# Performance work log

Hardware: AMD Instinct MI355X
Metric: run time of the kernel (lower is better)

The kernel has to match this reference:

```python
import jax, jax.numpy as jnp
import numpy as np

D_MODEL = 768
D_INNER = 1536   # expand=2
D_STATE = 16
D_CONV = 4
DT_RANK = 48     # ceil(768/16)
B, T, N = 2, 4, 196


def _rmsnorm(x, w, eps=1e-5):
    var = jnp.mean(x * x, axis=-1, keepdims=True)
    return x * jax.lax.rsqrt(var + eps) * w


def _causal_dwconv(x, w, b):
    # x: (b, l, di), w: (di, k) depthwise, causal left-pad k-1
    xc = jnp.swapaxes(x, 1, 2)  # (b, di, l)
    out = jax.lax.conv_general_dilated(
        xc, w[:, None, :], window_strides=(1,), padding=[(D_CONV - 1, 0)],
        feature_group_count=D_INNER, dimension_numbers=('NCH', 'OIH', 'NCH'))
    return jnp.swapaxes(out + b[None, :, None], 1, 2)


def _selective_scan(u, dt, A, Bm, Cm, Dp):
    # u, dt: (b,l,di); Bm, Cm: (b,l,n); A: (di,n); Dp: (di,)
    dA = jnp.exp(dt[..., None] * A)                    # (b,l,di,n)
    dBu = (dt * u)[..., None] * Bm[:, :, None, :]      # (b,l,di,n)

    def step(h, inp):
        dA_t, dBu_t, C_t = inp
        h = dA_t * h + dBu_t                           # (b,di,n)
        return h, jnp.einsum('bdn,bn->bd', h, C_t)

    h0 = jnp.zeros((u.shape[0], D_INNER, D_STATE), u.dtype)
    _, ys = jax.lax.scan(step, h0, (jnp.swapaxes(dA, 0, 1),
                                    jnp.swapaxes(dBu, 0, 1),
                                    jnp.swapaxes(Cm, 0, 1)))
    return jnp.swapaxes(ys, 0, 1) + u * Dp


def _mamba(x, in_w, cw, cb, xp_w, dt_w, dt_b, A_log, Dp, out_w):
    xz = jnp.einsum('blc,ec->ble', x, in_w)            # (b,l,2*di)
    xb, z = jnp.split(xz, 2, axis=-1)
    xb = jax.nn.silu(_causal_dwconv(xb, cw, cb))
    x_dbl = jnp.einsum('bld,ed->ble', xb, xp_w)        # (b,l,dt_rank+2n)
    dt, Bm, Cm = jnp.split(x_dbl, [DT_RANK, DT_RANK + D_STATE], axis=-1)
    dt = jax.nn.softplus(jnp.einsum('blr,dr->bld', dt, dt_w) + dt_b)
    y = _selective_scan(xb, dt, -jnp.exp(A_log), Bm, Cm, Dp)
    y = y * jax.nn.silu(z)
    return jnp.einsum('bld,cd->blc', y, out_w)


def _block(x, i, norm_w, in_proj_w, conv_w, conv_b, x_proj_w, dt_proj_w,
           dt_proj_b, A_log, D, mix_out_w):
    # residual Mamba block: x + mixer(norm(x)); zero-initialized ssm/conv state
    return x + _mamba(_rmsnorm(x, norm_w[i]), in_proj_w[i], conv_w[i], conv_b[i],
                      x_proj_w[i], dt_proj_w[i], dt_proj_b[i], A_log[i], D[i],
                      mix_out_w[i])


def _bimamba(x, norm_w, in_proj_w, conv_w, conv_b, x_proj_w, dt_proj_w,
             dt_proj_b, A_log, D, mix_out_w, gate_w, gate_b, proj_w, proj_b):
    b, t, n, c = x.shape
    xs = x.reshape(b, t * n, c)
    params = (norm_w, in_proj_w, conv_w, conv_b, x_proj_w, dt_proj_w,
              dt_proj_b, A_log, D, mix_out_w)
    out_f = _block(xs, 0, *params)
    flip_t = lambda y: y.reshape(b, t, n, c)[:, ::-1].reshape(b, t * n, c)
    out_b = flip_t(_block(flip_t(xs), 1, *params))
    gate = jax.nn.sigmoid(
        jnp.einsum('blc,dc->bld', jnp.concatenate([out_f, out_b], -1), gate_w)
        + gate_b)
    out = gate * out_f + (1.0 - gate) * out_b
    out = jnp.einsum('bld,cd->blc', out, proj_w) + proj_b
    return out.reshape(b, t, n, c)


def setup_inputs() -> dict:
    key = jax.random.key(0)
    ks = jax.random.split(key, 12)
    s = 0.02
    a_log = jnp.broadcast_to(
        jnp.log(jnp.arange(1, D_STATE + 1, dtype=jnp.float32)),
        (2, D_INNER, D_STATE)).copy()
    return {
        'x': jax.random.normal(ks[0], (B, T, N, D_MODEL), jnp.float32),
        'norm_w': jnp.ones((2, D_MODEL), jnp.float32),
        'in_proj_w': jax.random.normal(ks[1], (2, 2 * D_INNER, D_MODEL), jnp.float32) * s,
        'conv_w': jax.random.normal(ks[2], (2, D_INNER, D_CONV), jnp.float32) * 0.2,
        'conv_b': jnp.zeros((2, D_INNER), jnp.float32),
        'x_proj_w': jax.random.normal(ks[3], (2, DT_RANK + 2 * D_STATE, D_INNER), jnp.float32) * s,
        'dt_proj_w': jax.random.normal(ks[4], (2, D_INNER, DT_RANK), jnp.float32) * s,
        'dt_proj_b': jax.random.normal(ks[5], (2, D_INNER), jnp.float32) * 0.5 - 4.0,
        'A_log': a_log,
        'D': jnp.ones((2, D_INNER), jnp.float32),
        'mix_out_w': jax.random.normal(ks[6], (2, D_MODEL, D_INNER), jnp.float32) * s,
        'gate_w': jax.random.normal(ks[7], (D_MODEL, 2 * D_MODEL), jnp.float32) * s,
        'gate_b': jnp.zeros((D_MODEL,), jnp.float32),
        'proj_w': jax.random.normal(ks[8], (D_MODEL, D_MODEL), jnp.float32) * s,
        'proj_b': jnp.zeros((D_MODEL,), jnp.float32),
    }


def reference(x, norm_w, in_proj_w, conv_w, conv_b, x_proj_w, dt_proj_w,
              dt_proj_b, A_log, D, mix_out_w, gate_w, gate_b, proj_w, proj_b):
    return _bimamba(x, norm_w, in_proj_w, conv_w, conv_b, x_proj_w, dt_proj_w,
                    dt_proj_b, A_log, D, mix_out_w, gate_w, gate_b, proj_w,
                    proj_b)
```

## Files before the change

kernel.cpp:

```cpp
#include <hip/hip_runtime.h>
#include <cstdint>
#include <cstddef>

#define BB 2
#define TT 4
#define NN 196
#define LL (TT*NN)
#define BLr (BB*LL)
#define CM 768
#define DI 1536
#define DS 16
#define DTR 48
#define XD 80
#define GCH 16
#define LC (LL/GCH)
#define NST (2*BB*DI*DS)

typedef short s16x8 __attribute__((ext_vector_type(8)));
typedef float f32x4 __attribute__((ext_vector_type(4)));

static __device__ __forceinline__ float sigmoidf_(float x) {
  return 1.f / (1.f + __expf(-x));
}
static __device__ __forceinline__ unsigned short f2bf(float f) {
  unsigned int u = __float_as_uint(f);
  unsigned int r = (u + 0x7fffu + ((u >> 16) & 1u)) >> 16;
  return (unsigned short)r;
}
static __device__ __forceinline__ float bf2f(unsigned short u) {
  return __uint_as_float(((unsigned int)u) << 16);
}
static __device__ __forceinline__ float softplusf_(float v) {
  return (v > 20.f) ? v : __logf(1.f + __expf(v));
}
static __device__ __forceinline__ void gload_lds16(const void* g, void* l) {
  __builtin_amdgcn_global_load_lds(
      (const __attribute__((address_space(1))) void*)g,
      (__attribute__((address_space(3))) void*)l, 16, 0, 0);
}

__global__ __launch_bounds__(256) void rmsnorm_k(const float* __restrict__ x,
    const float* __restrict__ nw, unsigned short* __restrict__ xn)
{
  int blk = blockIdx.x;
  int l   = blk % LL;
  int b   = (blk / LL) % BB;
  int dir = blk / (BB*LL);
  int lsrc = l;
  if (dir == 1) { int t = l / NN, n = l % NN; lsrc = (TT-1-t)*NN + n; }
  const float* xp = x + ((size_t)b*LL + lsrc)*CM;
  float s = 0.f;
  for (int c = threadIdx.x; c < CM; c += 256) { float v = xp[c]; s += v*v; }
  #pragma unroll
  for (int off = 32; off > 0; off >>= 1) s += __shfl_down(s, off);
  __shared__ float red[4];
  if ((threadIdx.x & 63) == 0) red[threadIdx.x >> 6] = s;
  __syncthreads();
  float tot = red[0] + red[1] + red[2] + red[3];
  float r = rsqrtf(tot * (1.f/CM) + 1e-5f);
  const float* w = nw + dir*CM;
  unsigned short* o = xn + (size_t)blk*CM;
  for (int c = threadIdx.x; c < CM; c += 256) o[c] = f2bf(xp[c] * r * w[c]);
}

#define S_INW  4718592
#define S_OUTW 2359296
#define S_GATW 1179648
#define S_PRJW 589824
#define S_XPW  245760
#define S_DTW  196608
#define E0 S_INW
#define E1 (E0 + S_OUTW)
#define E2 (E1 + S_GATW)
#define E3 (E2 + S_PRJW)
#define E4 (E3 + S_XPW)
#define E5 (E4 + S_DTW)
__global__ void multicast_k(const float* __restrict__ in_w,
    const float* __restrict__ out_w, const float* __restrict__ gate_w,
    const float* __restrict__ proj_w, const float* __restrict__ xp_w,
    const float* __restrict__ dt_w, unsigned short* __restrict__ dst)
{
  int i = blockIdx.x*256 + threadIdx.x;
  if (i >= E5) return;
  float v;
  if (i < E0)       v = in_w[i];
  else if (i < E1)  v = out_w[i - E0];
  else if (i < E2)  v = gate_w[i - E1];
  else if (i < E3)  v = proj_w[i - E2];
  else if (i < E4)  v = xp_w[i - E3];
  else {
    int j = i - E4, r = j >> 6, c = j & 63;
    v = (c < 48) ? dt_w[r*48 + c] : 0.f;
  }
  dst[i] = f2bf(v);
}

template <int BM, int BN>
__device__ __forceinline__ void gemm_core(
    const unsigned short* __restrict__ A, int lda,
    const unsigned short* __restrict__ W, int ldw,
    int M, int N, int K, int m0, int n0,
    short* As, short* Ws, f32x4 (*acc)[BN/32])
{
  const int tid = threadIdx.x;
  const int wv = tid >> 6, lane = tid & 63;
  const int wm0 = (wv >> 1)*(BM/2), wn0 = (wv & 1)*(BN/2);
  const int lm = lane & 15, g = lane >> 4;
  const int r8 = lane >> 3, ch = lane & 7;
  const int chs = ch ^ r8;
  constexpr int MT = BM/32, NT = BN/32;
  for (int k0 = 0; k0 < K; k0 += 64) {
    #pragma unroll
    for (int e = 0; e < BM/32; ++e) {
      int rb = e*32 + wv*8;
      int gr = m0 + rb + r8; if (gr >= M) gr = M - 1;
      gload_lds16(A + (size_t)gr*lda + k0 + chs*8, &As[rb*64 + lane*8]);
    }
    #pragma unroll
    for (int e = 0; e < BN/32; ++e) {
      int rb = e*32 + wv*8;
      int gn = n0 + rb + r8; if (gn >= N) gn = N - 1;
      gload_lds16(W + (size_t)gn*ldw + k0 + chs*8, &Ws[rb*64 + lane*8]);
    }
    __syncthreads();
    #pragma unroll
    for (int s = 0; s < 2; ++s) {
      s16x8 af[MT], bf[NT];
      #pragma unroll
      for (int i = 0; i < MT; ++i) {
        int R = wm0 + i*16 + lm;
        af[i] = *(const s16x8*)(&As[R*64 + (((s*4 + g) ^ (R & 7))*8)]);
      }
      #pragma unroll
      for (int j = 0; j < NT; ++j) {
        int Rn = wn0 + j*16 + lm;
        bf[j] = *(const s16x8*)(&Ws[Rn*64 + (((s*4 + g) ^ (Rn & 7))*8)]);
      }
      #pragma unroll
      for (int i = 0; i < MT; ++i)
        #pragma unroll
        for (int j = 0; j < NT; ++j)
          acc[i][j] = __builtin_amdgcn_mfma_f32_16x16x32_bf16(af[i], bf[j], acc[i][j], 0, 0, 0);
    }
    __syncthreads();
  }
}

__global__ __launch_bounds__(256, 4) void gemm_in_k(
    const unsigned short* __restrict__ xn, const unsigned short* __restrict__ w,
    unsigned short* __restrict__ xzout)
{
  __shared__ short As[64*64];
  __shared__ short Ws[128*64];
  const int dir = blockIdx.z;
  const unsigned short* A = xn + (size_t)dir*BLr*CM;
  const unsigned short* W = w  + (size_t)dir*2*DI*CM;
  unsigned short* C = xzout + (size_t)dir*BLr*2*DI;
  const int m0 = blockIdx.y*64, n0 = blockIdx.x*128;
  f32x4 acc[2][4];
  #pragma unroll
  for (int i = 0; i < 2; ++i)
    #pragma unroll
    for (int j = 0; j < 4; ++j) acc[i][j] = (f32x4){0.f,0.f,0.f,0.f};
  gemm_core<64,128>(A, CM, W, CM, BLr, 2*DI, CM, m0, n0, As, Ws, acc);
  const int tid = threadIdx.x, wv = tid >> 6, lane = tid & 63;
  const int wm0 = (wv >> 1)*32, wn0 = (wv & 1)*64;
  const int lm = lane & 15, g = lane >> 4;
  #pragma unroll
  for (int i = 0; i < 2; ++i) {
    int row = m0 + wm0 + i*16 + g*4;
    #pragma unroll
    for (int j = 0; j < 4; ++j) {
      int col = n0 + wn0 + j*16 + lm;
      #pragma unroll
      for (int r = 0; r < 4; ++r)
        if (row + r < BLr) C[(size_t)(row + r)*2*DI + col] = f2bf(acc[i][j][r]);
    }
  }
}

__global__ __launch_bounds__(256, 4) void gemm_dt_k(
    const unsigned short* __restrict__ xdblb, const unsigned short* __restrict__ w,
    const float* __restrict__ dtb, float* __restrict__ dtv)
{
  __shared__ short As[64*64];
  __shared__ short Ws[128*64];
  const int dir = blockIdx.z;
  const unsigned short* A = xdblb + (size_t)dir*BLr*64;
  const unsigned short* W = w + (size_t)dir*DI*64;
  float* C = dtv + (size_t)dir*BLr*DI;
  const float* bias = dtb + (size_t)dir*DI;
  const int m0 = blockIdx.y*64, n0 = blockIdx.x*128;
  f32x4 acc[2][4];
  #pragma unroll
  for (int i = 0; i < 2; ++i)
    #pragma unroll
    for (int j = 0; j < 4; ++j) acc[i][j] = (f32x4){0.f,0.f,0.f,0.f};
  gemm_core<64,128>(A, 64, W, 64, BLr, DI, 64, m0, n0, As, Ws, acc);
  const int tid = threadIdx.x, wv = tid >> 6, lane = tid & 63;
  const int wm0 = (wv >> 1)*32, wn0 = (wv & 1)*64;
  const int lm = lane & 15, g = lane >> 4;
  #pragma unroll
  for (int i = 0; i < 2; ++i) {
    int row = m0 + wm0 + i*16 + g*4;
    #pragma unroll
    for (int j = 0; j < 4; ++j) {
      int col = n0 + wn0 + j*16 + lm;
      float bv = bias[col];
      #pragma unroll
      for (int r = 0; r < 4; ++r) {
        if (row + r >= BLr) continue;
        C[(size_t)(row + r)*DI + col] = softplusf_(acc[i][j][r] + bv);
      }
    }
  }
}

__global__ __launch_bounds__(256, 4) void gemm_outp_k(
    const unsigned short* __restrict__ yb, const unsigned short* __restrict__ w,
    const float* __restrict__ x, float* __restrict__ fbuf,
    float* __restrict__ bbuf, unsigned short* __restrict__ cat)
{
  __shared__ short As[64*64];
  __shared__ short Ws[64*64];
  const int dir = blockIdx.z;
  const unsigned short* A = yb + (size_t)dir*BLr*DI;
  const unsigned short* W = w + (size_t)dir*CM*DI;
  const int m0 = blockIdx.y*64, n0 = blockIdx.x*64;
  f32x4 acc[2][2];
  #pragma unroll
  for (int i = 0; i < 2; ++i)
    #pragma unroll
    for (int j = 0; j < 2; ++j) acc[i][j] = (f32x4){0.f,0.f,0.f,0.f};
  gemm_core<64,64>(A, DI, W, DI, BLr, CM, DI, m0, n0, As, Ws, acc);
  const int tid = threadIdx.x, wv = tid >> 6, lane = tid & 63;
  const int wm0 = (wv >> 1)*32, wn0 = (wv & 1)*32;
  const int lm = lane & 15, g = lane >> 4;
  #pragma unroll
  for (int i = 0; i < 2; ++i) {
    int row = m0 + wm0 + i*16 + g*4;
    #pragma unroll
    for (int j = 0; j < 2; ++j) {
      int col = n0 + wn0 + j*16 + lm;
      #pragma unroll
      for (int r = 0; r < 4; ++r) {
        int rr = row + r;
        if (rr >= BLr) continue;
        int rt = rr;
        if (dir == 1) {
          int l = rr % LL, b = rr / LL;
          int t = l / NN, nn = l % NN;
          rt = b*LL + (TT-1-t)*NN + nn;
        }
        float v = x[(size_t)rt*CM + col] + acc[i][j][r];
        if (dir == 0) {
          fbuf[(size_t)rt*CM + col] = v;
          cat[(size_t)rt*(2*CM) + col] = f2bf(v);
        } else {
          bbuf[(size_t)rt*CM + col] = v;
          cat[(size_t)rt*(2*CM) + CM + col] = f2bf(v);
        }
      }
    }
  }
}

__global__ __launch_bounds__(256, 4) void gemm_gate_k(
    const unsigned short* __restrict__ cat, const unsigned short* __restrict__ w,
    const float* __restrict__ gb, const float* __restrict__ fbuf,
    const float* __restrict__ bbuf, unsigned short* __restrict__ mixb)
{
  __shared__ short As[64*64];
  __shared__ short Ws[64*64];
  const int m0 = blockIdx.y*64, n0 = blockIdx.x*64;
  f32x4 acc[2][2];
  #pragma unroll
  for (int i = 0; i < 2; ++i)
    #pragma unroll
    for (int j = 0; j < 2; ++j) acc[i][j] = (f32x4){0.f,0.f,0.f,0.f};
  gemm_core<64,64>(cat, 2*CM, w, 2*CM, BLr, CM, 2*CM, m0, n0, As, Ws, acc);
  const int tid = threadIdx.x, wv = tid >> 6, lane = tid & 63;
  const int wm0 = (wv >> 1)*32, wn0 = (wv & 1)*32;
  const int lm = lane & 15, g = lane >> 4;
  #pragma unroll
  for (int i = 0; i < 2; ++i) {
    int row = m0 + wm0 + i*16 + g*4;
    #pragma unroll
    for (int j = 0; j < 2; ++j) {
      int col = n0 + wn0 + j*16 + lm;
      float bv = gb[col];
      #pragma unroll
      for (int r = 0; r < 4; ++r) {
        int rr = row + r;
        if (rr >= BLr) continue;
        float gg = sigmoidf_(acc[i][j][r] + bv);
        float fv = fbuf[(size_t)rr*CM + col];
        float bo = bbuf[(size_t)rr*CM + col];
        mixb[(size_t)rr*CM + col] = f2bf(gg*fv + (1.f - gg)*bo);
      }
    }
  }
}

__global__ __launch_bounds__(256, 4) void gemm_proj_k(
    const unsigned short* __restrict__ mixb, const unsigned short* __restrict__ w,
    const float* __restrict__ pb, float* __restrict__ out)
{
  __shared__ short As[64*64];
  __shared__ short Ws[64*64];
  const int m0 = blockIdx.y*64, n0 = blockIdx.x*64;
  f32x4 acc[2][2];
  #pragma unroll
  for (int i = 0; i < 2; ++i)
    #pragma unroll
    for (int j = 0; j < 2; ++j) acc[i][j] = (f32x4){0.f,0.f,0.f,0.f};
  gemm_core<64,64>(mixb, CM, w, CM, BLr, CM, CM, m0, n0, As, Ws, acc);
  const int tid = threadIdx.x, wv = tid >> 6, lane = tid & 63;
  const int wm0 = (wv >> 1)*32, wn0 = (wv & 1)*32;
  const int lm = lane & 15, g = lane >> 4;
  #pragma unroll
  for (int i = 0; i < 2; ++i) {
    int row = m0 + wm0 + i*16 + g*4;
    #pragma unroll
    for (int j = 0; j < 2; ++j) {
      int col = n0 + wn0 + j*16 + lm;
      float bv = pb[col];
      #pragma unroll
      for (int r = 0; r < 4; ++r)
        if (row + r < BLr) out[(size_t)(row + r)*CM + col] = acc[i][j][r] + bv;
    }
  }
}

__global__ __launch_bounds__(256, 2) void gemm_xproj(
    const unsigned short* __restrict__ ub, const unsigned short* __restrict__ xpw,
    float* __restrict__ part)
{
  __shared__ short As[128*64];
  __shared__ short Ws[128*64];
  const int ks = blockIdx.x, mt = blockIdx.y, dir = blockIdx.z;
  const unsigned short* A = ub + (size_t)dir*BLr*DI + ks*(DI/8);
  const unsigned short* W = xpw + (size_t)dir*XD*DI + ks*(DI/8);
  const int m0 = mt*128;
  f32x4 acc[4][4];
  #pragma unroll
  for (int i = 0; i < 4; ++i)
    #pragma unroll
    for (int j = 0; j < 4; ++j) acc[i][j] = (f32x4){0.f,0.f,0.f,0.f};
  gemm_core<128,128>(A, DI, W, DI, BLr, XD, DI/8, m0, 0, As, Ws, acc);
  const int tid = threadIdx.x, wv = tid >> 6, lane = tid & 63;
  const int wm0 = (wv >> 1)*64, wn0 = (wv & 1)*64;
  const int lm = lane & 15, g = lane >> 4;
  float* P = part + ((size_t)(dir*8 + ks)*BLr)*XD;
  #pragma unroll
  for (int i = 0; i < 4; ++i) {
    int row = m0 + wm0 + i*16 + g*4;
    #pragma unroll
    for (int j = 0; j < 4; ++j) {
      int col = wn0 + j*16 + lm;
      if (col >= XD) continue;
      #pragma unroll
      for (int r = 0; r < 4; ++r)
        if (row + r < BLr) P[(size_t)(row + r)*XD + col] = acc[i][j][r];
    }
  }
}

__global__ void xreduce_k(const float* __restrict__ part,
    float* __restrict__ xdbl, unsigned short* __restrict__ xdbl_b)
{
  int i = blockIdx.x*256 + threadIdx.x;
  if (i >= 2*BLr*XD) return;
  int c = i % XD;
  int r = i / XD;
  int dir = r / BLr, row = r % BLr;
  float s = 0.f;
  #pragma unroll
  for (int ks = 0; ks < 8; ++ks)
    s += part[((size_t)(dir*8 + ks)*BLr + row)*XD + c];
  xdbl[(size_t)r*XD + c] = s;
  if (c < DTR)      xdbl_b[(size_t)r*64 + c] = f2bf(s);
  else if (c < 64)  xdbl_b[(size_t)r*64 + c] = 0;
}

__global__ __launch_bounds__(256) void conv_silu_k(
    const unsigned short* __restrict__ xz, const float* __restrict__ cw,
    const float* __restrict__ cb, unsigned short* __restrict__ ub)
{
  size_t idx = (size_t)blockIdx.x*256 + threadIdx.x;
  if (idx >= (size_t)2*BLr*DI) return;
  int di  = (int)(idx % DI);
  size_t r = idx / DI;
  int l   = (int)(r % LL);
  int dir = (int)(r / (BB*LL));
  size_t rowbase = r - l;
  const float* w = cw + ((size_t)dir*DI + di)*4;
  float acc = cb[dir*DI + di];
  #pragma unroll
  for (int k = 0; k < 4; ++k) {
    int lp = l - 3 + k;
    if (lp >= 0) acc = fmaf(w[k], bf2f(xz[(rowbase + lp)*(2*DI) + di]), acc);
  }
  float v = acc * sigmoidf_(acc);
  ub[idx] = f2bf(v);
}

__global__ __launch_bounds__(256) void scanA_k(const float* __restrict__ dtv,
    const unsigned short* __restrict__ u, const float* __restrict__ xdbl,
    const float* __restrict__ A_log, float* __restrict__ carry,
    float* __restrict__ Pm)
{
  int bx = blockIdx.x;
  int g = bx & (GCH-1);
  int rest = bx / GCH;
  int dchunk = rest % (DI/64);
  int b   = (rest / (DI/64)) % BB;
  int dir = rest / ((DI/64)*BB);
  int tid = threadIdx.x;
  int dl = tid >> 2, q = tid & 3;
  int d = dchunk*64 + dl;
  size_t rb = ((size_t)dir*BB + b) * LL + (size_t)g*LC;
  const float* dtp = dtv + rb*DI + d;
  const unsigned short* up = u + rb*DI + d;
  const float* xB  = xdbl + rb*XD + DTR + 4*q;
  f32x4 al = *(const f32x4*)(A_log + ((size_t)dir*DI + d)*DS + 4*q);
  float Av[4];
  #pragma unroll
  for (int i = 0; i < 4; ++i) Av[i] = -__expf(al[i]);
  float h[4] = {0.f,0.f,0.f,0.f};
  float S = 0.f;
  float ndt[2], nu[2]; f32x4 nB[2];
  #pragma unroll
  for (int e = 0; e < 2; ++e) {
    ndt[e] = dtp[(size_t)e*DI];
    nu[e]  = bf2f(up[(size_t)e*DI]);
    nB[e]  = *(const f32x4*)(xB + (size_t)e*XD);
  }
  #pragma unroll 2
  for (int j = 0; j < LC; ++j) {
    int s = j & 1;
    float cdt = ndt[s], cu = nu[s];
    f32x4 cB = nB[s];
    int lp = j + 2;
    if (lp < LC) {
      ndt[s] = dtp[(size_t)lp*DI];
      nu[s]  = bf2f(up[(size_t)lp*DI]);
      nB[s]  = *(const f32x4*)(xB + (size_t)lp*XD);
    }
    float du = cdt * cu;
    S += cdt;
    #pragma unroll
    for (int i = 0; i < 4; ++i) {
      float dA = __expf(cdt * Av[i]);
      h[i] = fmaf(dA, h[i], du * cB[i]);
    }
  }
  size_t sid = (((size_t)(dir*BB + b)*DI + d)*DS + 4*q);
  f32x4 hc = {h[0], h[1], h[2], h[3]};
  f32x4 pc = {__expf(Av[0]*S), __expf(Av[1]*S), __expf(Av[2]*S), __expf(Av[3]*S)};
  *(f32x4*)(carry + (size_t)g*NST + sid) = hc;
  *(f32x4*)(Pm    + (size_t)g*NST + sid) = pc;
}

__global__ __launch_bounds__(256) void scanB_k(float* __restrict__ carry,
    const float* __restrict__ Pm)
{
  int sid = blockIdx.x*256 + threadIdx.x;
  float h = 0.f;
  #pragma unroll
  for (int g = 0; g < GCH; ++g) {
    float c = carry[(size_t)g*NST + sid];
    float p = Pm[(size_t)g*NST + sid];
    carry[(size_t)g*NST + sid] = h;
    h = fmaf(p, h, c);
  }
}

__global__ __launch_bounds__(256) void scanC_k(const float* __restrict__ dtv,
    const unsigned short* __restrict__ u, const unsigned short* __restrict__ xz,
    const float* __restrict__ xdbl, const float* __restrict__ A_log,
    const float* __restrict__ Dp, const float* __restrict__ h_in,
    unsigned short* __restrict__ y)
{
  int bx = blockIdx.x;
  int g = bx & (GCH-1);
  int rest = bx / GCH;
  int dchunk = rest % (DI/64);
  int b   = (rest / (DI/64)) % BB;
  int dir = rest / ((DI/64)*BB);
  int tid = threadIdx.x;
  int dl = tid >> 2, q = tid & 3;
  int d = dchunk*64 + dl;
  size_t rb = ((size_t)dir*BB + b) * LL + (size_t)g*LC;
  const float* dtp = dtv + rb*DI + d;
  const unsigned short* up = u + rb*DI + d;
  const unsigned short* zp = xz + rb*(2*DI) + DI + d;
  const float* xB  = xdbl + rb*XD + DTR + 4*q;
  const float* xC  = xB + DS;
  unsigned short* yp = y + rb*DI + d;
  f32x4 al = *(const f32x4*)(A_log + ((size_t)dir*DI + d)*DS + 4*q);
  float Av[4];
  #pragma unroll
  for (int i = 0; i < 4; ++i) Av[i] = -__expf(al[i]);
  float Dd = Dp[dir*DI + d];
  size_t sid = (((size_t)(dir*BB + b)*DI + d)*DS + 4*q);
  f32x4 h4 = *(const f32x4*)(h_in + (size_t)g*NST + sid);
  float h[4] = {h4[0], h4[1], h4[2], h4[3]};
  float ndt[2], nu[2], nz[2]; f32x4 nB[2], nC[2];
  #pragma unroll
  for (int e = 0; e < 2; ++e) {
    ndt[e] = dtp[(size_t)e*DI];
    nu[e]  = bf2f(up[(size_t)e*DI]);
    nz[e]  = bf2f(zp[(size_t)e*(2*DI)]);
    nB[e]  = *(const f32x4*)(xB + (size_t)e*XD);
    nC[e]  = *(const f32x4*)(xC + (size_t)e*XD);
  }
  #pragma unroll 2
  for (int j = 0; j < LC; ++j) {
    int s = j & 1;
    float cdt = ndt[s], cu = nu[s], cz = nz[s];
    f32x4 cB = nB[s], cC = nC[s];
    int lp = j + 2;
    if (lp < LC) {
      ndt[s] = dtp[(size_t)lp*DI];
      nu[s]  = bf2f(up[(size_t)lp*DI]);
      nz[s]  = bf2f(zp[(size_t)lp*(2*DI)]);
      nB[s]  = *(const f32x4*)(xB + (size_t)lp*XD);
      nC[s]  = *(const f32x4*)(xC + (size_t)lp*XD);
    }
    float du = cdt * cu;
    float acc = 0.f;
    #pragma unroll
    for (int i = 0; i < 4; ++i) {
      float dA = __expf(cdt * Av[i]);
      h[i] = fmaf(dA, h[i], du * cB[i]);
      acc = fmaf(h[i], cC[i], acc);
    }
    acc += __shfl_xor(acc, 1);
    acc += __shfl_xor(acc, 2);
    if (q == 0) {
      float yv = (acc + cu * Dd) * (cz * sigmoidf_(cz));
      yp[(size_t)j*DI] = f2bf(yv);
    }
  }
}

extern "C" void kernel_launch(void* const* d_in, const int* in_sizes, int n_in,
                              void* d_out, int out_size, void* d_ws, size_t ws_size,
                              hipStream_t stream)
{
  (void)in_sizes; (void)n_in; (void)out_size; (void)ws_size;
  const float* x      = (const float*)d_in[0];
  const float* norm_w = (const float*)d_in[1];
  const float* in_w   = (const float*)d_in[2];
  const float* conv_w = (const float*)d_in[3];
  const float* conv_b = (const float*)d_in[4];
  const float* xp_w   = (const float*)d_in[5];
  const float* dt_w   = (const float*)d_in[6];
  const float* dt_b   = (const float*)d_in[7];
  const float* A_log  = (const float*)d_in[8];
  const float* Dp     = (const float*)d_in[9];
  const float* out_w  = (const float*)d_in[10];
  const float* gate_w = (const float*)d_in[11];
  const float* gate_b = (const float*)d_in[12];
  const float* proj_w = (const float*)d_in[13];
  const float* proj_b = (const float*)d_in[14];
  float* out = (float*)d_out;
  char* wsb  = (char*)d_ws;

  unsigned short* w_all   = (unsigned short*)(wsb + 0);
  unsigned short* in_w_b  = w_all;
  unsigned short* out_w_b = w_all + E0;
  unsigned short* gate_w_b= w_all + E1;
  unsigned short* proj_w_b= w_all + E2;
  unsigned short* xp_w_b  = w_all + E3;
  unsigned short* dt_w_b  = w_all + E4;
  unsigned short* xz_b = (unsigned short*)(wsb + 18579456);
  unsigned short* ub   = (unsigned short*)(wsb + 37847040);
  float* xdbl  = (float*)(wsb + 57114624);
  float* dtvb  = (float*)(wsb + 58118144);
  unsigned short* y_b = (unsigned short*)(wsb + 77385728);
  unsigned short* tmp = (unsigned short*)(wsb + 87019520);
  float* fbuf  = (float*)(wsb + 96653312);
  float* bbuf  = (float*)(wsb + 101470208);
  unsigned short* cat_b = (unsigned short*)(wsb + 106287104);
  unsigned short* mix_b = (unsigned short*)(wsb + 111104000);

  unsigned short* xn_b   = tmp;
  unsigned short* xdbl_b = tmp;
  float* part  = (float*)(wsb + 0);
  float* carry = (float*)(wsb + 0);
  float* Pmat  = (float*)(wsb + 87019520 + 524288);

  rmsnorm_k<<<2*BLr, 256, 0, stream>>>(x, norm_w, xn_b);
  multicast_k<<<(E5 + 255)/256, 256, 0, stream>>>(
      in_w, out_w, gate_w, proj_w, xp_w, dt_w, w_all);
  gemm_in_k<<<dim3(3072/128, (BLr+63)/64, 2), 256, 0, stream>>>(
      xn_b, in_w_b, xz_b);
  conv_silu_k<<<(int)(((size_t)2*BLr*DI + 255)/256), 256, 0, stream>>>(
      xz_b, conv_w, conv_b, ub);
  gemm_xproj<<<dim3(8, (BLr+127)/128, 2), 256, 0, stream>>>(ub, xp_w_b, part);
  xreduce_k<<<(2*BLr*XD + 255)/256, 256, 0, stream>>>(part, xdbl, xdbl_b);
  gemm_dt_k<<<dim3(DI/128, (BLr+63)/64, 2), 256, 0, stream>>>(
      xdbl_b, dt_w_b, dt_b, dtvb);
  scanA_k<<<2*BB*(DI/64)*GCH, 256, 0, stream>>>(
      dtvb, ub, xdbl, A_log, carry, Pmat);
  scanB_k<<<NST/256, 256, 0, stream>>>(carry, Pmat);
  scanC_k<<<2*BB*(DI/64)*GCH, 256, 0, stream>>>(
      dtvb, ub, xz_b, xdbl, A_log, Dp, carry, y_b);
  gemm_outp_k<<<dim3(CM/64, (BLr+63)/64, 2), 256, 0, stream>>>(
      y_b, out_w_b, x, fbuf, bbuf, cat_b);
  gemm_gate_k<<<dim3(CM/64, (BLr+63)/64, 1), 256, 0, stream>>>(
      cat_b, gate_w_b, gate_b, fbuf, bbuf, mix_b);
  gemm_proj_k<<<dim3(CM/64, (BLr+63)/64, 1), 256, 0, stream>>>(
      mix_b, proj_w_b, proj_b, out);
}
```

Baseline: 310.0 us.

## Fuse rmsnorm with weight cast, enlarge GEMM tiles, drop fp32 residual buffers

Merges the rmsnorm and weight bf16-cast kernels into one launch. Grows the in-projection GEMM tile to 128x128 with launch bounds lowered to 2, and widens the out-projection tile to 64x128. Removes the fp32 forward/backward residual buffers, so the gate kernel reads the bf16 concatenated values instead. That cuts memory traffic and a launch, but the gating now uses bf16-rounded branch outputs, a small precision change.

Measured after the change: 310.2 us. Within noise of the previous version (+0.1%).

```diff
diff --git a/kernel.cpp b/kernel.cpp
--- a/kernel.cpp
+++ b/kernel.cpp
@@ -39,30 +39,6 @@
       (__attribute__((address_space(3))) void*)l, 16, 0, 0);
 }
 
-__global__ __launch_bounds__(256) void rmsnorm_k(const float* __restrict__ x,
-    const float* __restrict__ nw, unsigned short* __restrict__ xn)
-{
-  int blk = blockIdx.x;
-  int l   = blk % LL;
-  int b   = (blk / LL) % BB;
-  int dir = blk / (BB*LL);
-  int lsrc = l;
-  if (dir == 1) { int t = l / NN, n = l % NN; lsrc = (TT-1-t)*NN + n; }
-  const float* xp = x + ((size_t)b*LL + lsrc)*CM;
-  float s = 0.f;
-  for (int c = threadIdx.x; c < CM; c += 256) { float v = xp[c]; s += v*v; }
-  #pragma unroll
-  for (int off = 32; off > 0; off >>= 1) s += __shfl_down(s, off);
-  __shared__ float red[4];
-  if ((threadIdx.x & 63) == 0) red[threadIdx.x >> 6] = s;
-  __syncthreads();
-  float tot = red[0] + red[1] + red[2] + red[3];
-  float r = rsqrtf(tot * (1.f/CM) + 1e-5f);
-  const float* w = nw + dir*CM;
-  unsigned short* o = xn + (size_t)blk*CM;
-  for (int c = threadIdx.x; c < CM; c += 256) o[c] = f2bf(xp[c] * r * w[c]);
-}
-
 #define S_INW  4718592
 #define S_OUTW 2359296
 #define S_GATW 1179648
@@ -75,24 +51,49 @@
 #define E3 (E2 + S_PRJW)
 #define E4 (E3 + S_XPW)
 #define E5 (E4 + S_DTW)
-__global__ void multicast_k(const float* __restrict__ in_w,
-    const float* __restrict__ out_w, const float* __restrict__ gate_w,
-    const float* __restrict__ proj_w, const float* __restrict__ xp_w,
-    const float* __restrict__ dt_w, unsigned short* __restrict__ dst)
-{
-  int i = blockIdx.x*256 + threadIdx.x;
-  if (i >= E5) return;
-  float v;
-  if (i < E0)       v = in_w[i];
-  else if (i < E1)  v = out_w[i - E0];
-  else if (i < E2)  v = gate_w[i - E1];
-  else if (i < E3)  v = proj_w[i - E2];
-  else if (i < E4)  v = xp_w[i - E3];
-  else {
-    int j = i - E4, r = j >> 6, c = j & 63;
-    v = (c < 48) ? dt_w[r*48 + c] : 0.f;
-  }
-  dst[i] = f2bf(v);
+#define NCAST ((E5)/256)
+
+__global__ __launch_bounds__(256) void pre_k(const float* __restrict__ x,
+    const float* __restrict__ nw, unsigned short* __restrict__ xn,
+    const float* __restrict__ in_w, const float* __restrict__ out_w,
+    const float* __restrict__ gate_w, const float* __restrict__ proj_w,
+    const float* __restrict__ xp_w, const float* __restrict__ dt_w,
+    unsigned short* __restrict__ dst)
+{
+  int blk = blockIdx.x;
+  if (blk < 2*BLr) {
+    int l   = blk % LL;
+    int b   = (blk / LL) % BB;
+    int dir = blk / (BB*LL);
+    int lsrc = l;
+    if (dir == 1) { int t = l / NN, n = l % NN; lsrc = (TT-1-t)*NN + n; }
+    const float* xp = x + ((size_t)b*LL + lsrc)*CM;
+    float s = 0.f;
+    for (int c = threadIdx.x; c < CM; c += 256) { float v = xp[c]; s += v*v; }
+    #pragma unroll
+    for (int off = 32; off > 0; off >>= 1) s += __shfl_down(s, off);
+    __shared__ float red[4];
+    if ((threadIdx.x & 63) == 0) red[threadIdx.x >> 6] = s;
+    __syncthreads();
+    float tot = red[0] + red[1] + red[2] + red[3];
+    float r = rsqrtf(tot * (1.f/CM) + 1e-5f);
+    const float* w = nw + dir*CM;
+    unsigned short* o = xn + (size_t)blk*CM;
+    for (int c = threadIdx.x; c < CM; c += 256) o[c] = f2bf(xp[c] * r * w[c]);
+  } else {
+    int i = (blk - 2*BLr)*256 + threadIdx.x;
+    float v;
+    if (i < E0)       v = in_w[i];
+    else if (i < E1)  v = out_w[i - E0];
+    else if (i < E2)  v = gate_w[i - E1];
+    else if (i < E3)  v = proj_w[i - E2];
+    else if (i < E4)  v = xp_w[i - E3];
+    else {
+      int j = i - E4, r = j >> 6, c = j & 63;
+      v = (c < 48) ? dt_w[r*48 + c] : 0.f;
+    }
+    dst[i] = f2bf(v);
+  }
 }
 
 template <int BM, int BN>
@@ -146,28 +147,28 @@
   }
 }
 
-__global__ __launch_bounds__(256, 4) void gemm_in_k(
+__global__ __launch_bounds__(256, 2) void gemm_in_k(
     const unsigned short* __restrict__ xn, const unsigned short* __restrict__ w,
     unsigned short* __restrict__ xzout)
 {
-  __shared__ short As[64*64];
+  __shared__ short As[128*64];
   __shared__ short Ws[128*64];
   const int dir = blockIdx.z;
   const unsigned short* A = xn + (size_t)dir*BLr*CM;
   const unsigned short* W = w  + (size_t)dir*2*DI*CM;
   unsigned short* C = xzout + (size_t)dir*BLr*2*DI;
-  const int m0 = blockIdx.y*64, n0 = blockIdx.x*128;
-  f32x4 acc[2][4];
-  #pragma unroll
-  for (int i = 0; i < 2; ++i)
+  const int m0 = blockIdx.y*128, n0 = blockIdx.x*128;
+  f32x4 acc[4][4];
+  #pragma unroll
+  for (int i = 0; i < 4; ++i)
     #pragma unroll
     for (int j = 0; j < 4; ++j) acc[i][j] = (f32x4){0.f,0.f,0.f,0.f};
-  gemm_core<64,128>(A, CM, W, CM, BLr, 2*DI, CM, m0, n0, As, Ws, acc);
+  gemm_core<128,128>(A, CM, W, CM, BLr, 2*DI, CM, m0, n0, As, Ws, acc);
   const int tid = threadIdx.x, wv = tid >> 6, lane = tid & 63;
-  const int wm0 = (wv >> 1)*32, wn0 = (wv & 1)*64;
+  const int wm0 = (wv >> 1)*64, wn0 = (wv & 1)*64;
   const int lm = lane & 15, g = lane >> 4;
   #pragma unroll
-  for (int i = 0; i < 2; ++i) {
+  for (int i = 0; i < 4; ++i) {
     int row = m0 + wm0 + i*16 + g*4;
     #pragma unroll
     for (int j = 0; j < 4; ++j) {
@@ -218,29 +219,28 @@
 
 __global__ __launch_bounds__(256, 4) void gemm_outp_k(
     const unsigned short* __restrict__ yb, const unsigned short* __restrict__ w,
-    const float* __restrict__ x, float* __restrict__ fbuf,
-    float* __restrict__ bbuf, unsigned short* __restrict__ cat)
+    const float* __restrict__ x, unsigned short* __restrict__ cat)
 {
   __shared__ short As[64*64];
-  __shared__ short Ws[64*64];
+  __shared__ short Ws[128*64];
   const int dir = blockIdx.z;
   const unsigned short* A = yb + (size_t)dir*BLr*DI;
   const unsigned short* W = w + (size_t)dir*CM*DI;
-  const int m0 = blockIdx.y*64, n0 = blockIdx.x*64;
-  f32x4 acc[2][2];
+  const int m0 = blockIdx.y*64, n0 = blockIdx.x*128;
+  f32x4 acc[2][4];
   #pragma unroll
   for (int i = 0; i < 2; ++i)
     #pragma unroll
-    for (int j = 0; j < 2; ++j) acc[i][j] = (f32x4){0.f,0.f,0.f,0.f};
-  gemm_core<64,64>(A, DI, W, DI, BLr, CM, DI, m0, n0, As, Ws, acc);
+    for (int j = 0; j < 4; ++j) acc[i][j] = (f32x4){0.f,0.f,0.f,0.f};
+  gemm_core<64,128>(A, DI, W, DI, BLr, CM, DI, m0, n0, As, Ws, acc);
   const int tid = threadIdx.x, wv = tid >> 6, lane = tid & 63;
-  const int wm0 = (wv >> 1)*32, wn0 = (wv & 1)*32;
+  const int wm0 = (wv >> 1)*32, wn0 = (wv & 1)*64;
   const int lm = lane & 15, g = lane >> 4;
   #pragma unroll
   for (int i = 0; i < 2; ++i) {
     int row = m0 + wm0 + i*16 + g*4;
     #pragma unroll
-    for (int j = 0; j < 2; ++j) {
+    for (int j = 0; j < 4; ++j) {
       int col = n0 + wn0 + j*16 + lm;
       #pragma unroll
       for (int r = 0; r < 4; ++r) {
@@ -253,13 +253,7 @@
           rt = b*LL + (TT-1-t)*NN + nn;
         }
         float v = x[(size_t)rt*CM + col] + acc[i][j][r];
-        if (dir == 0) {
-          fbuf[(size_t)rt*CM + col] = v;
-          cat[(size_t)rt*(2*CM) + col] = f2bf(v);
-        } else {
-          bbuf[(size_t)rt*CM + col] = v;
-          cat[(size_t)rt*(2*CM) + CM + col] = f2bf(v);
-        }
+        cat[(size_t)rt*(2*CM) + dir*CM + col] = f2bf(v);
       }
     }
   }
@@ -267,8 +261,7 @@
 
 __global__ __launch_bounds__(256, 4) void gemm_gate_k(
     const unsigned short* __restrict__ cat, const unsigned short* __restrict__ w,
-    const float* __restrict__ gb, const float* __restrict__ fbuf,
-    const float* __restrict__ bbuf, unsigned short* __restrict__ mixb)
+    const float* __restrict__ gb, unsigned short* __restrict__ mixb)
 {
   __shared__ short As[64*64];
   __shared__ short Ws[64*64];
@@ -294,8 +287,8 @@
         int rr = row + r;
         if (rr >= BLr) continue;
         float gg = sigmoidf_(acc[i][j][r] + bv);
-        float fv = fbuf[(size_t)rr*CM + col];
-        float bo = bbuf[(size_t)rr*CM + col];
+        float fv = bf2f(cat[(size_t)rr*(2*CM) + col]);
+        float bo = bf2f(cat[(size_t)rr*(2*CM) + CM + col]);
         mixb[(size_t)rr*CM + col] = f2bf(gg*fv + (1.f - gg)*bo);
       }
     }
@@ -373,8 +366,8 @@
   if (i >= 2*BLr*XD) return;
   int c = i % XD;
   int r = i / XD;
+  float s = 0.f;
   int dir = r / BLr, row = r % BLr;
-  float s = 0.f;
   #pragma unroll
   for (int ks = 0; ks < 8; ++ks)
     s += part[((size_t)(dir*8 + ks)*BLr + row)*XD + c];
@@ -581,8 +574,6 @@
   float* dtvb  = (float*)(wsb + 58118144);
   unsigned short* y_b = (unsigned short*)(wsb + 77385728);
   unsigned short* tmp = (unsigned short*)(wsb + 87019520);
-  float* fbuf  = (float*)(wsb + 96653312);
-  float* bbuf  = (float*)(wsb + 101470208);
   unsigned short* cat_b = (unsigned short*)(wsb + 106287104);
   unsigned short* mix_b = (unsigned short*)(wsb + 111104000);
 
@@ -592,10 +583,9 @@
   float* carry = (float*)(wsb + 0);
   float* Pmat  = (float*)(wsb + 87019520 + 524288);
 
-  rmsnorm_k<<<2*BLr, 256, 0, stream>>>(x, norm_w, xn_b);
-  multicast_k<<<(E5 + 255)/256, 256, 0, stream>>>(
-      in_w, out_w, gate_w, proj_w, xp_w, dt_w, w_all);
-  gemm_in_k<<<dim3(3072/128, (BLr+63)/64, 2), 256, 0, stream>>>(
+  pre_k<<<2*BLr + NCAST, 256, 0, stream>>>(
+      x, norm_w, xn_b, in_w, out_w, gate_w, proj_w, xp_w, dt_w, w_all);
+  gemm_in_k<<<dim3(3072/128, (BLr+127)/128, 2), 256, 0, stream>>>(
       xn_b, in_w_b, xz_b);
   conv_silu_k<<<(int)(((size_t)2*BLr*DI + 255)/256), 256, 0, stream>>>(
       xz_b, conv_w, conv_b, ub);
@@ -608,10 +598,10 @@
   scanB_k<<<NST/256, 256, 0, stream>>>(carry, Pmat);
   scanC_k<<<2*BB*(DI/64)*GCH, 256, 0, stream>>>(
       dtvb, ub, xz_b, xdbl, A_log, Dp, carry, y_b);
-  gemm_outp_k<<<dim3(CM/64, (BLr+63)/64, 2), 256, 0, stream>>>(
-      y_b, out_w_b, x, fbuf, bbuf, cat_b);
+  gemm_outp_k<<<dim3(CM/128, (BLr+63)/64, 2), 256, 0, stream>>>(
+      y_b, out_w_b, x, cat_b);
   gemm_gate_k<<<dim3(CM/64, (BLr+63)/64, 1), 256, 0, stream>>>(
-      cat_b, gate_w_b, gate_b, fbuf, bbuf, mix_b);
+      cat_b, gate_w_b, gate_b, mix_b);
   gemm_proj_k<<<dim3(CM/64, (BLr+63)/64, 1), 256, 0, stream>>>(
       mix_b, proj_w_b, proj_b, out);
 }
```
